# Kernel optimization log

Measured on AMD Instinct MI355X. Metric: run time of the kernel, lower is better.

## Reference

```python
import jax, jax.numpy as jnp
import numpy as np

B, PATCH, S, D, LAYERS, TOP_K, N_HEADS = 32, 196, 77, 512, 2, 16, 8


def setup_inputs() -> dict:
    key = jax.random.key(0)
    ks = jax.random.split(key, 16)
    d, L = D, LAYERS
    attn_std = d ** -0.5
    proj_std = (d ** -0.5) * ((2 * L) ** -0.5)
    fc_std = (2 * d) ** -0.5
    scale = d ** -0.5
    f = jnp.float32
    return {
        'image_feature': jax.random.normal(ks[0], (B, d), f),
        'image_tokens': jax.random.normal(ks[1], (B, PATCH, d), f),
        'text_feature': jax.random.normal(ks[2], (B, d), f),
        'text_tokens': jax.random.normal(ks[3], (B, S, d), f),
        'atte_mask': jax.random.randint(ks[4], (B, S), 0, 2).astype(jnp.int32),
        'img_cls': scale * jax.random.normal(ks[5], (d,), f),
        'txt_cls': scale * jax.random.normal(ks[6], (d,), f),
        'in_proj_w': attn_std * jax.random.normal(ks[7], (L, 3 * d, d), f),
        'in_proj_b': jnp.zeros((L, 3 * d), f),
        'out_w': proj_std * jax.random.normal(ks[8], (L, d, d), f),
        'out_b': jnp.zeros((L, d), f),
        'ln1_w': jnp.ones((L, d), f), 'ln1_b': jnp.zeros((L, d), f),
        'ln2_w': jnp.ones((L, d), f), 'ln2_b': jnp.zeros((L, d), f),
        'ln3_w': jnp.ones((L, d), f), 'ln3_b': jnp.zeros((L, d), f),
        'fc_w': fc_std * jax.random.normal(ks[9], (L, 4 * d, d), f),
        'fc_b': jnp.zeros((L, 4 * d), f),
        'proj_w': proj_std * jax.random.normal(ks[10], (L, d, 4 * d), f),
        'proj_b': jnp.zeros((L, d), f),
    }


def _ln(x, w, b):
    m = jnp.mean(x, axis=-1, keepdims=True)
    v = jnp.mean((x - m) ** 2, axis=-1, keepdims=True)
    return (x - m) * jax.lax.rsqrt(v + 1e-5) * w + b


def _mha(q, k, wi, bi, wo, bo):
    # q: (N, Lq, d), k: (N, Lk, d)
    N, Lq, d = q.shape
    hd = d // N_HEADS
    qh = (q @ wi[:d].T + bi[:d]).reshape(N, Lq, N_HEADS, hd)
    kh = (k @ wi[d:2 * d].T + bi[d:2 * d]).reshape(N, -1, N_HEADS, hd)
    vh = (k @ wi[2 * d:].T + bi[2 * d:]).reshape(N, -1, N_HEADS, hd)
    att = jax.nn.softmax(jnp.einsum('bqhd,bkhd->bhqk', qh, kh) * (hd ** -0.5), axis=-1)
    o = jnp.einsum('bhqk,bkhd->bqhd', att, vh).reshape(N, Lq, d)
    return o @ wo.T + bo


def _cross_attention(q4, k4, p):
    shape4 = q4.shape
    q = q4.reshape(-1, q4.shape[-2], q4.shape[-1])
    k = k4.reshape(-1, k4.shape[-2], k4.shape[-1])
    for i in range(LAYERS):
        kn = _ln(k, p['ln2_w'][i], p['ln2_b'][i])
        q = q + _mha(_ln(q, p['ln1_w'][i], p['ln1_b'][i]), kn,
                     p['in_proj_w'][i], p['in_proj_b'][i], p['out_w'][i], p['out_b'][i])
        h = _ln(q, p['ln3_w'][i], p['ln3_b'][i]) @ p['fc_w'][i].T + p['fc_b'][i]
        h = h * jax.nn.sigmoid(1.702 * h)  # QuickGELU
        q = q + h @ p['proj_w'][i].T + p['proj_b'][i]
    return q.reshape(shape4)


def _forward(image_feature, image_tokens, text_feature, text_tokens, atte_mask,
             img_cls, txt_cls, p):
    b, patch, d = image_tokens.shape
    s = text_tokens.shape[1]
    img_n = image_tokens / jnp.linalg.norm(image_tokens, axis=-1, keepdims=True)
    txt_n = text_tokens / jnp.linalg.norm(text_tokens, axis=-1, keepdims=True)
    # pairwise token similarities: (b_img, b_txt, patch, s)
    sim = jnp.einsum('ipd,jsd->ijps', img_n, txt_n)
    img_scores = jnp.einsum('ijps,js->ijp', sim, atte_mask.astype(sim.dtype))
    txt_scores = sim.sum(axis=2)  # (b, b, s)
    # top-k; torch scatter+masked_select gathers in ascending index order
    idx_i = jnp.sort(jax.lax.top_k(img_scores, TOP_K)[1], axis=-1)  # (b,b,k)
    idx_t = jnp.sort(jax.lax.top_k(txt_scores, TOP_K)[1], axis=-1)
    img_sel = img_n[jnp.arange(b)[:, None, None], idx_i]  # (b,b,k,d)
    txt_sel = txt_n[jnp.arange(b)[None, :, None], idx_t]  # (b,b,k,d)
    img_feat = jnp.broadcast_to(image_feature[:, None, None, :], (b, b, 1, d))
    txt_feat = jnp.broadcast_to(text_feature[None, :, None, :], (b, b, 1, d))
    img_cls4 = jnp.broadcast_to(img_cls, (b, b, 1, d))
    txt_cls4 = jnp.broadcast_to(txt_cls, (b, b, 1, d))
    final_img = _cross_attention(jnp.concatenate([img_cls4, img_sel], axis=2),
                                 jnp.concatenate([txt_feat, txt_sel], axis=2), p)
    final_txt = _cross_attention(jnp.concatenate([txt_cls4, txt_sel], axis=2),
                                 jnp.concatenate([img_feat, img_sel], axis=2), p)
    return final_img, final_txt


def reference(image_feature, image_tokens, text_feature, text_tokens, atte_mask,
              img_cls, txt_cls, in_proj_w, in_proj_b, out_w, out_b,
              ln1_w, ln1_b, ln2_w, ln2_b, ln3_w, ln3_b,
              fc_w, fc_b, proj_w, proj_b):
    p = dict(in_proj_w=in_proj_w, in_proj_b=in_proj_b, out_w=out_w, out_b=out_b,
             ln1_w=ln1_w, ln1_b=ln1_b, ln2_w=ln2_w, ln2_b=ln2_b,
             ln3_w=ln3_w, ln3_b=ln3_b, fc_w=fc_w, fc_b=fc_b,
             proj_w=proj_w, proj_b=proj_b)
    return _forward(image_feature, image_tokens, text_feature, text_tokens,
                    atte_mask, img_cls, txt_cls, p)
```

## Files before the change

kernel.cpp:

```cpp
#include <hip/hip_runtime.h>
#include <hip/hip_bf16.h>
#include <stdint.h>


typedef __attribute__((ext_vector_type(8))) short short8;
typedef __attribute__((ext_vector_type(4))) float f32x4;

__device__ __forceinline__ float bf2f(short u) {
    return __uint_as_float(((uint32_t)(uint16_t)u) << 16);
}
__device__ __forceinline__ unsigned short f2bf(float f) {
    __hip_bfloat16 h = __float2bfloat16(f);
    return *reinterpret_cast<unsigned short*>(&h);
}
__device__ __forceinline__ void gload16(const void* g, void* l) {
    __builtin_amdgcn_global_load_lds(
        (const __attribute__((address_space(1))) unsigned int*)g,
        (__attribute__((address_space(3))) unsigned int*)l, 16, 0, 0);
}

__global__ __launch_bounds__(256) void k_f2b(const float* __restrict__ in,
                                             unsigned short* __restrict__ out, int n) {
    for (int i = blockIdx.x * 256 + threadIdx.x; i < n; i += gridDim.x * 256)
        out[i] = f2bf(in[i]);
}

__global__ __launch_bounds__(256) void k_l2norm(const float* __restrict__ in,
                                                float* __restrict__ out) {
    size_t row = blockIdx.x;
    const float* x = in + row * 512;
    int t = threadIdx.x;
    float a0 = x[t], a1 = x[t + 256];
    float ss = a0 * a0 + a1 * a1;
#pragma unroll
    for (int off = 32; off; off >>= 1) ss += __shfl_xor(ss, off);
    __shared__ float s4[4];
    if ((t & 63) == 0) s4[t >> 6] = ss;
    __syncthreads();
    float tot = s4[0] + s4[1] + s4[2] + s4[3];
    float inv = 1.0f / sqrtf(tot);
    out[row * 512 + t] = a0 * inv;
    out[row * 512 + t + 256] = a1 * inv;
}

__global__ __launch_bounds__(512) void k_colsum(const float* __restrict__ tok,
                                                const int* __restrict__ mask,
                                                float* __restrict__ out, int R) {
    int b = blockIdx.x;
    int d = threadIdx.x;
    float acc = 0.f;
    for (int r = 0; r < R; r++) {
        float m = mask ? (float)mask[b * R + r] : 1.f;
        acc += m * tok[((size_t)b * R + r) * 512 + d];
    }
    out[b * 512 + d] = acc;
}

__global__ __launch_bounds__(256) void k_scores(const float* __restrict__ tok,
                                                const float* __restrict__ vec,
                                                float* __restrict__ out, int R, int swap) {
    int bid = blockIdx.x;
    int i = bid >> 5, j = bid & 31;
    int tb = swap ? j : i;
    int vb = swap ? i : j;
    __shared__ float sv[512];
    for (int t = threadIdx.x; t < 512; t += 256) sv[t] = vec[vb * 512 + t];
    __syncthreads();
    int wv = threadIdx.x >> 6, lane = threadIdx.x & 63;
    for (int r = wv; r < R; r += 4) {
        const float* tr = tok + ((size_t)tb * R + r) * 512;
        float acc = 0.f;
#pragma unroll
        for (int c = 0; c < 8; c++) {
            int d = lane + c * 64;
            acc += tr[d] * sv[d];
        }
#pragma unroll
        for (int off = 32; off; off >>= 1) acc += __shfl_xor(acc, off);
        if (lane == 0) out[(size_t)bid * R + r] = acc;
    }
}

__global__ __launch_bounds__(64) void k_topk(const float* __restrict__ simg,
                                             const float* __restrict__ stxt,
                                             int* __restrict__ idx_i, int* __restrict__ idx_t) {
    int bid = blockIdx.x;
    bool isimg = bid < 1024;
    int ij = isimg ? bid : bid - 1024;
    const float* s = isimg ? simg + (size_t)ij * 196 : stxt + (size_t)ij * 77;
    int n = isimg ? 196 : 77;
    int* out = (isimg ? idx_i : idx_t) + ij * 16;
    int lane = threadIdx.x;
    float v[4];
    int ids[4];
#pragma unroll
    for (int k = 0; k < 4; k++) {
        int id = lane + k * 64;
        ids[k] = id;
        v[k] = (id < n) ? s[id] : -3.0e38f;
    }
    __shared__ int sel[16];
    for (int r = 0; r < 16; r++) {
        float bv = v[0];
        int bi = ids[0];
#pragma unroll
        for (int k = 1; k < 4; k++)
            if (v[k] > bv) { bv = v[k]; bi = ids[k]; }
#pragma unroll
        for (int off = 32; off; off >>= 1) {
            float ov = __shfl_xor(bv, off);
            int oi = __shfl_xor(bi, off);
            if (ov > bv || (ov == bv && oi < bi)) { bv = ov; bi = oi; }
        }
        if (lane == 0) sel[r] = bi;
#pragma unroll
        for (int k = 0; k < 4; k++)
            if (ids[k] == bi) v[k] = -3.0e38f;
    }
    if (lane == 0) {
        for (int a = 1; a < 16; a++) {
            int key = sel[a];
            int b = a - 1;
            while (b >= 0 && sel[b] > key) { sel[b + 1] = sel[b]; b--; }
            sel[b + 1] = key;
        }
        for (int a = 0; a < 16; a++) out[a] = sel[a];
    }
}

__global__ __launch_bounds__(128) void k_gather(const float* __restrict__ img_n,
                                                const float* __restrict__ txt_n,
                                                const float* __restrict__ img_feat,
                                                const float* __restrict__ txt_feat,
                                                const float* __restrict__ img_cls,
                                                const float* __restrict__ txt_cls,
                                                const int* __restrict__ idx_i,
                                                const int* __restrict__ idx_t,
                                                float* __restrict__ q,
                                                unsigned short* __restrict__ k) {
    int rid = blockIdx.x;
    int buf = rid / 34816;
    int rem = rid % 34816;
    int seq = rem / 17, t = rem % 17;
    int c = seq >> 10, ij = seq & 1023, i = ij >> 5, j = ij & 31;
    const float* src;
    if (buf == 0) {
        if (c == 0)
            src = (t == 0) ? img_cls : img_n + ((size_t)i * 196 + idx_i[ij * 16 + t - 1]) * 512;
        else
            src = (t == 0) ? txt_cls : txt_n + ((size_t)j * 77 + idx_t[ij * 16 + t - 1]) * 512;
    } else {
        if (c == 0)
            src = (t == 0) ? (txt_feat + (size_t)j * 512)
                           : txt_n + ((size_t)j * 77 + idx_t[ij * 16 + t - 1]) * 512;
        else
            src = (t == 0) ? (img_feat + (size_t)i * 512)
                           : img_n + ((size_t)i * 196 + idx_i[ij * 16 + t - 1]) * 512;
    }
    float4 v = ((const float4*)src)[threadIdx.x];
    size_t row = (size_t)seq * 17 + t;
    if (buf == 0) {
        ((float4*)(q + row * 512))[threadIdx.x] = v;
    } else {
        ushort4 o;
        o.x = f2bf(v.x); o.y = f2bf(v.y); o.z = f2bf(v.z); o.w = f2bf(v.w);
        ((ushort4*)(k + row * 512))[threadIdx.x] = o;
    }
}

template <int BF>
__global__ __launch_bounds__(256) void k_ln(const void* __restrict__ xv,
                                            const float* __restrict__ w,
                                            const float* __restrict__ b,
                                            unsigned short* __restrict__ out) {
    size_t row = blockIdx.x;
    int t = threadIdx.x;
    float a0, a1;
    if (BF) {
        const short* xr = (const short*)xv + row * 512;
        a0 = bf2f(xr[t]);
        a1 = bf2f(xr[t + 256]);
    } else {
        const float* xr = (const float*)xv + row * 512;
        a0 = xr[t];
        a1 = xr[t + 256];
    }
    float s = a0 + a1, qq = a0 * a0 + a1 * a1;
#pragma unroll
    for (int off = 32; off; off >>= 1) {
        s += __shfl_xor(s, off);
        qq += __shfl_xor(qq, off);
    }
    __shared__ float s4[4], q4[4];
    if ((t & 63) == 0) { s4[t >> 6] = s; q4[t >> 6] = qq; }
    __syncthreads();
    s = s4[0] + s4[1] + s4[2] + s4[3];
    qq = q4[0] + q4[1] + q4[2] + q4[3];
    float mean = s * (1.f / 512.f);
    float var = qq * (1.f / 512.f) - mean * mean;
    float rs = rsqrtf(var + 1e-5f);
    out[row * 512 + t] = f2bf((a0 - mean) * rs * w[t] + b[t]);
    out[row * 512 + t + 256] = f2bf((a1 - mean) * rs * w[t + 256] + b[t + 256]);
}

template <int MODE>
__global__ __launch_bounds__(256) void k_gemm(const unsigned short* __restrict__ A,
                                              const unsigned short* __restrict__ W,
                                              const float* __restrict__ bias,
                                              void* __restrict__ Cv, int K, int ldc, int nxt) {
    __shared__ __align__(16) short sU[2][8192];

    int nwg = gridDim.x;
    int orig = blockIdx.x;
    int q8 = nwg >> 3, r8 = nwg & 7;
    int xcd = orig & 7, base = orig >> 3;
    int swz = (xcd < r8 ? xcd * (q8 + 1) : r8 * (q8 + 1) + (xcd - r8) * q8) + base;
    int tn = swz % nxt, tm = swz / nxt;

    int tid = threadIdx.x;
    int lane = tid & 63;
    int w = tid >> 6;
    int wm = w >> 1, wn = w & 1;
    int r16 = lane & 15, g = lane >> 4;

    int srow = tid >> 2;
    int sgran = tid & 3;
    int gchunk = (sgran ^ ((srow ^ (srow >> 2)) & 3)) * 8;
    const short* gA = (const short*)A + ((size_t)tm * 128 + srow) * K + gchunk;
    const short* gB = (const short*)W + ((size_t)tn * 128 + srow) * K + gchunk;
    int ldst = tid * 8;

    f32x4 acc[4][4] = {};
    int NU = K >> 5;

#define STAGE_UNIT(U, S)                                              \
    do {                                                              \
        size_t ko_ = (size_t)(U) * 32;                                \
        gload16(gA + ko_, &sU[(S)][ldst]);                            \
        gload16(gA + (size_t)64 * K + ko_, &sU[(S)][2048 + ldst]);    \
        gload16(gB + ko_, &sU[(S)][4096 + ldst]);                     \
        gload16(gB + (size_t)64 * K + ko_, &sU[(S)][6144 + ldst]);    \
    } while (0)

    STAGE_UNIT(0, 0);
    STAGE_UNIT(1, 1);

    int s = 0;
    for (int u = 0; u < NU; ++u) {
        if (u + 1 < NU) asm volatile("s_waitcnt vmcnt(4)" ::: "memory");
        else            asm volatile("s_waitcnt vmcnt(0)" ::: "memory");
        __builtin_amdgcn_s_barrier();
        __builtin_amdgcn_sched_barrier(0);

        const short* SA = &sU[s][0];
        const short* SB = &sU[s][4096];
        short8 a[4], b[4];
#pragma unroll
        for (int m = 0; m < 4; m++) {
            int row = wm * 64 + m * 16 + r16;
            a[m] = *(const short8*)&SA[row * 32 + ((g ^ ((row ^ (row >> 2)) & 3)) << 3)];
        }
#pragma unroll
        for (int n = 0; n < 4; n++) {
            int row = wn * 64 + n * 16 + r16;
            b[n] = *(const short8*)&SB[row * 32 + ((g ^ ((row ^ (row >> 2)) & 3)) << 3)];
        }
        __builtin_amdgcn_s_setprio(1);
#pragma unroll
        for (int m = 0; m < 4; m++)
#pragma unroll
            for (int n = 0; n < 4; n++)
                acc[m][n] = __builtin_amdgcn_mfma_f32_16x16x32_bf16(a[m], b[n], acc[m][n], 0, 0, 0);
        __builtin_amdgcn_s_setprio(0);
        __builtin_amdgcn_sched_barrier(0);
        __builtin_amdgcn_s_barrier();
        if (u + 2 < NU) STAGE_UNIT(u + 2, s);
        s ^= 1;
    }
#undef STAGE_UNIT

    size_t rbase = (size_t)tm * 128 + wm * 64 + g * 4;
    size_t cbase = (size_t)tn * 128 + wn * 64 + r16;
#pragma unroll
    for (int m = 0; m < 4; m++)
#pragma unroll
        for (int n = 0; n < 4; n++) {
            size_t col = cbase + n * 16;
            float bv = bias ? bias[col] : 0.f;
#pragma unroll
            for (int r = 0; r < 4; r++) {
                size_t row = rbase + m * 16 + r;
                float val = acc[m][n][r] + bv;
                if (MODE == 0) {
                    ((unsigned short*)Cv)[row * ldc + col] = f2bf(val);
                } else if (MODE == 1) {
                    float gv = val / (1.f + __expf(-1.702f * val));
                    ((unsigned short*)Cv)[row * ldc + col] = f2bf(gv);
                } else {
                    ((float*)Cv)[row * ldc + col] += val;
                }
            }
        }
}

__global__ __launch_bounds__(512) void k_attn(const unsigned short* __restrict__ Qm,
                                              const unsigned short* __restrict__ KVm,
                                              unsigned short* __restrict__ Om) {
    __shared__ __align__(16) short sAll[3 * 17 * 520];
    __shared__ float sP[8 * 17 * 17];
    int seq = blockIdx.x;
    size_t tb = (size_t)seq * 17;
    for (int c = threadIdx.x; c < 3264; c += 512) {
        int mat = c / 1088, rem = c % 1088, row = rem >> 6, ch = rem & 63;
        const short8* src;
        if (mat == 0)
            src = (const short8*)(Qm + (tb + row) * 512 + ch * 8);
        else if (mat == 1)
            src = (const short8*)(KVm + (tb + row) * 1024 + ch * 8);
        else
            src = (const short8*)(KVm + (tb + row) * 1024 + 512 + ch * 8);
        *(short8*)&sAll[mat * (17 * 520) + row * 520 + ch * 8] = *src;
    }
    __syncthreads();
    int h = threadIdx.x >> 6, lane = threadIdx.x & 63;
    const short* sQ = sAll;
    const short* sK = sAll + 17 * 520;
    const short* sV = sAll + 2 * 17 * 520;
    int jj = lane < 17 ? lane : 0;
    for (int i = 0; i < 17; i++) {
        float acc = 0.f;
#pragma unroll
        for (int c = 0; c < 8; c++) {
            short8 q8 = *(const short8*)&sQ[i * 520 + h * 64 + c * 8];
            short8 k8 = *(const short8*)&sK[jj * 520 + h * 64 + c * 8];
#pragma unroll
            for (int e = 0; e < 8; e++) acc += bf2f(q8[e]) * bf2f(k8[e]);
        }
        float sc = (lane < 17) ? acc * 0.125f : -1e30f;
        float m = sc;
#pragma unroll
        for (int off = 32; off; off >>= 1) m = fmaxf(m, __shfl_xor(m, off));
        float p = (lane < 17) ? __expf(sc - m) : 0.f;
        float sum = p;
#pragma unroll
        for (int off = 32; off; off >>= 1) sum += __shfl_xor(sum, off);
        if (lane < 17) sP[(h * 17 + i) * 17 + lane] = p / sum;
    }
    for (int i = 0; i < 17; i++) {
        float o = 0.f;
#pragma unroll
        for (int t = 0; t < 17; t++)
            o += sP[(h * 17 + i) * 17 + t] * bf2f(sV[t * 520 + h * 64 + lane]);
        Om[(tb + i) * 512 + h * 64 + lane] = f2bf(o);
    }
}

extern "C" void kernel_launch(void* const* d_in, const int* in_sizes, int n_in,
                              void* d_out, int out_size, void* d_ws, size_t ws_size,
                              hipStream_t stream) {
    const float* image_feature = (const float*)d_in[0];
    const float* image_tokens = (const float*)d_in[1];
    const float* text_feature = (const float*)d_in[2];
    const float* text_tokens = (const float*)d_in[3];
    const int* atte_mask = (const int*)d_in[4];
    const float* img_cls = (const float*)d_in[5];
    const float* txt_cls = (const float*)d_in[6];
    const float* in_proj_w = (const float*)d_in[7];
    const float* in_proj_b = (const float*)d_in[8];
    const float* out_w = (const float*)d_in[9];
    const float* out_b = (const float*)d_in[10];
    const float* ln1_w = (const float*)d_in[11];
    const float* ln1_b = (const float*)d_in[12];
    const float* ln2_w = (const float*)d_in[13];
    const float* ln2_b = (const float*)d_in[14];
    const float* ln3_w = (const float*)d_in[15];
    const float* ln3_b = (const float*)d_in[16];
    const float* fc_w = (const float*)d_in[17];
    const float* fc_b = (const float*)d_in[18];
    const float* proj_w = (const float*)d_in[19];
    const float* proj_b = (const float*)d_in[20];

    char* ws = (char*)d_ws;
    const size_t OFF_K = 12582912;
    const size_t OFF_CH = OFF_K + 35651584;
    size_t avail = ws_size > OFF_CH ? ws_size - OFF_CH : 0;
    int C = 2048;
    while (C > 256 && (size_t)87040 * C > avail) C >>= 1;
    int nch = 2048 / C;

    unsigned short* wbf = (unsigned short*)ws;
    unsigned short* w_inproj = wbf;
    unsigned short* w_outp = wbf + 1572864;
    unsigned short* w_fc = wbf + 2097152;
    unsigned short* w_proj = wbf + 4194304;
    unsigned short* kstream = (unsigned short*)(ws + OFF_K);
    char* chreg = ws + OFF_CH;
    float* img_n = (float*)(chreg + 0);
    float* txt_n = (float*)(chreg + 12845056);
    float* isum = (float*)(chreg + 17891328);
    float* tmask = (float*)(chreg + 17956864);
    float* simg = (float*)(chreg + 18022400);
    float* stxt = (float*)(chreg + 18825216);
    int* idx_i = (int*)(chreg + 19140608);
    int* idx_t = (int*)(chreg + 19206144);
    unsigned short* qn = (unsigned short*)chreg;
    unsigned short* qkvQ = (unsigned short*)(chreg + (size_t)17408 * C);
    unsigned short* qkvKV = (unsigned short*)(chreg + (size_t)34816 * C);
    unsigned short* atto = (unsigned short*)(chreg + (size_t)69632 * C);
    unsigned short* hbuf = qkvQ;
    float* q = (float*)d_out;

    k_f2b<<<1024, 256, 0, stream>>>(in_proj_w, w_inproj, 1572864);
    k_f2b<<<1024, 256, 0, stream>>>(out_w, w_outp, 524288);
    k_f2b<<<1024, 256, 0, stream>>>(fc_w, w_fc, 2097152);
    k_f2b<<<1024, 256, 0, stream>>>(proj_w, w_proj, 2097152);

    k_l2norm<<<6272, 256, 0, stream>>>(image_tokens, img_n);
    k_l2norm<<<2464, 256, 0, stream>>>(text_tokens, txt_n);

    k_colsum<<<32, 512, 0, stream>>>(img_n, nullptr, isum, 196);
    k_colsum<<<32, 512, 0, stream>>>(txt_n, atte_mask, tmask, 77);

    k_scores<<<1024, 256, 0, stream>>>(img_n, tmask, simg, 196, 0);
    k_scores<<<1024, 256, 0, stream>>>(txt_n, isum, stxt, 77, 1);
    k_topk<<<2048, 64, 0, stream>>>(simg, stxt, idx_i, idx_t);
    k_gather<<<69632, 128, 0, stream>>>(img_n, txt_n, image_feature, text_feature,
                                        img_cls, txt_cls, idx_i, idx_t, q, kstream);

    for (int ch = 0; ch < nch; ch++) {
        size_t r0 = (size_t)ch * C * 17;
        float* qc = q + r0 * 512;
        const unsigned short* kc = kstream + r0 * 512;
        int rowsC = 17 * C;
        int gmt = rowsC / 128;
        for (int l = 0; l < 2; l++) {
            const unsigned short* Wq = w_inproj + (size_t)l * 786432;
            const unsigned short* Wkv = Wq + 262144;
            const float* bq = in_proj_b + l * 1536;
            const float* bkv = bq + 512;
            k_ln<0><<<rowsC, 256, 0, stream>>>(qc, ln1_w + l * 512, ln1_b + l * 512, qn);
            k_gemm<0><<<gmt * 4, 256, 0, stream>>>(qn, Wq, bq, qkvQ, 512, 512, 4);
            k_ln<1><<<rowsC, 256, 0, stream>>>(kc, ln2_w + l * 512, ln2_b + l * 512, qn);
            k_gemm<0><<<gmt * 8, 256, 0, stream>>>(qn, Wkv, bkv, qkvKV, 512, 1024, 8);
            k_attn<<<C, 512, 0, stream>>>(qkvQ, qkvKV, atto);
            k_gemm<2><<<gmt * 4, 256, 0, stream>>>(atto, w_outp + (size_t)l * 262144,
                                                   out_b + l * 512, qc, 512, 512, 4);
            k_ln<0><<<rowsC, 256, 0, stream>>>(qc, ln3_w + l * 512, ln3_b + l * 512, qn);
            k_gemm<1><<<gmt * 16, 256, 0, stream>>>(qn, w_fc + (size_t)l * 1048576,
                                                    fc_b + l * 2048, hbuf, 512, 2048, 16);
            k_gemm<2><<<gmt * 4, 256, 0, stream>>>(hbuf, w_proj + (size_t)l * 1048576,
                                                   proj_b + l * 512, qc, 2048, 512, 4);
        }
    }
}
```

Baseline: 1.352 ms.

## Vectorize LayerNorm, stage bf16 GEMM epilogue through LDS, merge weight casts

LayerNorm now assigns one row per wavefront and reads and writes 8 elements per lane with vector loads. This drops the cross-wave LDS reduction and __syncthreads. The bf16 GEMM epilogues write the tile into LDS and then store it to global memory with coalesced 16-byte writes, replacing scattered 2-byte stores. The four weight-conversion launches are merged into one kernel. The LDS staging reuses the operand buffer after a barrier, which adds a sync and some LDS traffic. The LN row count must be divisible by 4.

```diff
diff --git a/kernel.cpp b/kernel.cpp
--- a/kernel.cpp
+++ b/kernel.cpp
@@ -19,10 +19,19 @@
         (__attribute__((address_space(3))) unsigned int*)l, 16, 0, 0);
 }
 
-__global__ __launch_bounds__(256) void k_f2b(const float* __restrict__ in,
-                                             unsigned short* __restrict__ out, int n) {
-    for (int i = blockIdx.x * 256 + threadIdx.x; i < n; i += gridDim.x * 256)
-        out[i] = f2bf(in[i]);
+__global__ __launch_bounds__(256) void k_f2b4(const float* __restrict__ s0,
+                                              const float* __restrict__ s1,
+                                              const float* __restrict__ s2,
+                                              const float* __restrict__ s3,
+                                              unsigned short* __restrict__ out) {
+    for (int i = blockIdx.x * 256 + threadIdx.x; i < 6291456; i += gridDim.x * 256) {
+        float v;
+        if (i < 1572864) v = s0[i];
+        else if (i < 2097152) v = s1[i - 1572864];
+        else if (i < 4194304) v = s2[i - 2097152];
+        else v = s3[i - 4194304];
+        out[i] = f2bf(v);
+    }
 }
 
 __global__ __launch_bounds__(256) void k_l2norm(const float* __restrict__ in,
@@ -173,34 +182,42 @@
                                             const float* __restrict__ w,
                                             const float* __restrict__ b,
                                             unsigned short* __restrict__ out) {
-    size_t row = blockIdx.x;
-    int t = threadIdx.x;
-    float a0, a1;
+    int wv = threadIdx.x >> 6, lane = threadIdx.x & 63;
+    size_t row = (size_t)blockIdx.x * 4 + wv;
+    float v[8];
     if (BF) {
-        const short* xr = (const short*)xv + row * 512;
-        a0 = bf2f(xr[t]);
-        a1 = bf2f(xr[t + 256]);
+        short8 x = *(const short8*)((const short*)xv + row * 512 + lane * 8);
+#pragma unroll
+        for (int e = 0; e < 8; e++) v[e] = bf2f(x[e]);
     } else {
-        const float* xr = (const float*)xv + row * 512;
-        a0 = xr[t];
-        a1 = xr[t + 256];
-    }
-    float s = a0 + a1, qq = a0 * a0 + a1 * a1;
+        const float* xr = (const float*)xv + row * 512 + lane * 8;
+        float4 x0 = *(const float4*)xr;
+        float4 x1 = *(const float4*)(xr + 4);
+        v[0] = x0.x; v[1] = x0.y; v[2] = x0.z; v[3] = x0.w;
+        v[4] = x1.x; v[5] = x1.y; v[6] = x1.z; v[7] = x1.w;
+    }
+    float s = 0.f, qq = 0.f;
+#pragma unroll
+    for (int e = 0; e < 8; e++) { s += v[e]; qq += v[e] * v[e]; }
 #pragma unroll
     for (int off = 32; off; off >>= 1) {
         s += __shfl_xor(s, off);
         qq += __shfl_xor(qq, off);
     }
-    __shared__ float s4[4], q4[4];
-    if ((t & 63) == 0) { s4[t >> 6] = s; q4[t >> 6] = qq; }
-    __syncthreads();
-    s = s4[0] + s4[1] + s4[2] + s4[3];
-    qq = q4[0] + q4[1] + q4[2] + q4[3];
     float mean = s * (1.f / 512.f);
     float var = qq * (1.f / 512.f) - mean * mean;
     float rs = rsqrtf(var + 1e-5f);
-    out[row * 512 + t] = f2bf((a0 - mean) * rs * w[t] + b[t]);
-    out[row * 512 + t + 256] = f2bf((a1 - mean) * rs * w[t + 256] + b[t + 256]);
+    const float* wr = w + lane * 8;
+    const float* br = b + lane * 8;
+    float4 w0 = *(const float4*)wr, w1 = *(const float4*)(wr + 4);
+    float4 b0 = *(const float4*)br, b1 = *(const float4*)(br + 4);
+    float wv8[8] = {w0.x, w0.y, w0.z, w0.w, w1.x, w1.y, w1.z, w1.w};
+    float bv8[8] = {b0.x, b0.y, b0.z, b0.w, b1.x, b1.y, b1.z, b1.w};
+    short8 res;
+#pragma unroll
+    for (int e = 0; e < 8; e++)
+        res[e] = (short)f2bf((v[e] - mean) * rs * wv8[e] + bv8[e]);
+    *(short8*)(out + row * 512 + lane * 8) = res;
 }
 
 template <int MODE>
@@ -279,28 +296,48 @@
     }
 #undef STAGE_UNIT
 
-    size_t rbase = (size_t)tm * 128 + wm * 64 + g * 4;
-    size_t cbase = (size_t)tn * 128 + wn * 64 + r16;
-#pragma unroll
-    for (int m = 0; m < 4; m++)
-#pragma unroll
-        for (int n = 0; n < 4; n++) {
-            size_t col = cbase + n * 16;
-            float bv = bias ? bias[col] : 0.f;
-#pragma unroll
-            for (int r = 0; r < 4; r++) {
-                size_t row = rbase + m * 16 + r;
-                float val = acc[m][n][r] + bv;
-                if (MODE == 0) {
-                    ((unsigned short*)Cv)[row * ldc + col] = f2bf(val);
-                } else if (MODE == 1) {
-                    float gv = val / (1.f + __expf(-1.702f * val));
-                    ((unsigned short*)Cv)[row * ldc + col] = f2bf(gv);
-                } else {
-                    ((float*)Cv)[row * ldc + col] += val;
+    if (MODE == 2) {
+        size_t rbase = (size_t)tm * 128 + wm * 64 + g * 4;
+        size_t cbase = (size_t)tn * 128 + wn * 64 + r16;
+#pragma unroll
+        for (int m = 0; m < 4; m++)
+#pragma unroll
+            for (int n = 0; n < 4; n++) {
+                size_t col = cbase + n * 16;
+                float bv = bias ? bias[col] : 0.f;
+#pragma unroll
+                for (int r = 0; r < 4; r++) {
+                    size_t row = rbase + m * 16 + r;
+                    ((float*)Cv)[row * ldc + col] += acc[m][n][r] + bv;
                 }
             }
-        }
+    } else {
+        short* sC = &sU[0][0];
+        int lrow = wm * 64 + g * 4;
+        int lcol = wn * 64 + r16;
+#pragma unroll
+        for (int n = 0; n < 4; n++) {
+            float bv = bias ? bias[(size_t)tn * 128 + lcol + n * 16] : 0.f;
+#pragma unroll
+            for (int m = 0; m < 4; m++)
+#pragma unroll
+                for (int r = 0; r < 4; r++) {
+                    float val = acc[m][n][r] + bv;
+                    if (MODE == 1) val = val / (1.f + __expf(-1.702f * val));
+                    sC[(lrow + m * 16 + r) * 128 + lcol + n * 16] = (short)f2bf(val);
+                }
+        }
+        __builtin_amdgcn_s_barrier();
+        unsigned short* C = (unsigned short*)Cv;
+#pragma unroll
+        for (int p = 0; p < 8; p++) {
+            int idx = p * 256 + tid;
+            int row = idx >> 4;
+            int cc = idx & 15;
+            *(short8*)(C + ((size_t)tm * 128 + row) * ldc + (size_t)tn * 128 + cc * 8) =
+                *(const short8*)&sC[row * 128 + cc * 8];
+        }
+    }
 }
 
 __global__ __launch_bounds__(512) void k_attn(const unsigned short* __restrict__ Qm,
@@ -410,10 +447,7 @@
     unsigned short* hbuf = qkvQ;
     float* q = (float*)d_out;
 
-    k_f2b<<<1024, 256, 0, stream>>>(in_proj_w, w_inproj, 1572864);
-    k_f2b<<<1024, 256, 0, stream>>>(out_w, w_outp, 524288);
-    k_f2b<<<1024, 256, 0, stream>>>(fc_w, w_fc, 2097152);
-    k_f2b<<<1024, 256, 0, stream>>>(proj_w, w_proj, 2097152);
+    k_f2b4<<<3072, 256, 0, stream>>>(in_proj_w, out_w, fc_w, proj_w, wbf);
 
     k_l2norm<<<6272, 256, 0, stream>>>(image_tokens, img_n);
     k_l2norm<<<2464, 256, 0, stream>>>(text_tokens, txt_n);
@@ -433,19 +467,20 @@
         const unsigned short* kc = kstream + r0 * 512;
         int rowsC = 17 * C;
         int gmt = rowsC / 128;
+        int gln = rowsC / 4;
         for (int l = 0; l < 2; l++) {
             const unsigned short* Wq = w_inproj + (size_t)l * 786432;
             const unsigned short* Wkv = Wq + 262144;
             const float* bq = in_proj_b + l * 1536;
             const float* bkv = bq + 512;
-            k_ln<0><<<rowsC, 256, 0, stream>>>(qc, ln1_w + l * 512, ln1_b + l * 512, qn);
+            k_ln<0><<<gln, 256, 0, stream>>>(qc, ln1_w + l * 512, ln1_b + l * 512, qn);
             k_gemm<0><<<gmt * 4, 256, 0, stream>>>(qn, Wq, bq, qkvQ, 512, 512, 4);
-            k_ln<1><<<rowsC, 256, 0, stream>>>(kc, ln2_w + l * 512, ln2_b + l * 512, qn);
+            k_ln<1><<<gln, 256, 0, stream>>>(kc, ln2_w + l * 512, ln2_b + l * 512, qn);
             k_gemm<0><<<gmt * 8, 256, 0, stream>>>(qn, Wkv, bkv, qkvKV, 512, 1024, 8);
             k_attn<<<C, 512, 0, stream>>>(qkvQ, qkvKV, atto);
             k_gemm<2><<<gmt * 4, 256, 0, stream>>>(atto, w_outp + (size_t)l * 262144,
                                                    out_b + l * 512, qc, 512, 512, 4);
-            k_ln<0><<<rowsC, 256, 0, stream>>>(qc, ln3_w + l * 512, ln3_b + l * 512, qn);
+            k_ln<0><<<gln, 256, 0, stream>>>(qc, ln3_w + l * 512, ln3_b + l * 512, qn);
             k_gemm<1><<<gmt * 16, 256, 0, stream>>>(qn, w_fc + (size_t)l * 1048576,
                                                     fc_b + l * 2048, hbuf, 512, 2048, 16);
             k_gemm<2><<<gmt * 4, 256, 0, stream>>>(hbuf, w_proj + (size_t)l * 1048576,
```

New measurement: 1.272 ms. 5.9% less time.
